# Kernel optimization log

Measured on AMD Instinct MI355X. Metric: run time of the kernel, lower is better.

The kernel has to match this reference:

```python
import jax, jax.numpy as jnp
import numpy as np

K = 3
STRIDE = 1
PAD = 1


def conv2d(x, w, b, stride, pad):
    y = jax.lax.conv_general_dilated(
        x, w, (stride, stride), [(pad, pad), (pad, pad)],
        dimension_numbers=("NCHW", "OIHW", "NCHW"))
    return y + b[None, :, None, None]


def setup_inputs() -> dict:
    key = jax.random.key(0)
    k1, k2, k3, k4, k5, k6 = jax.random.split(key, 6)
    B, C, H, W = 8, 128, 64, 64
    O = 128
    x = jax.random.normal(k1, (B, C, H, W), dtype=jnp.float32)
    # torch zero-inits offset/mask convs; use small random weights so the
    # deformable sampling path is actually exercised (offsets ~O(0.5) px).
    w_offset = jax.random.normal(k2, (2 * K * K, C, K, K), dtype=jnp.float32) * 0.02
    b_offset = jax.random.normal(k3, (2 * K * K,), dtype=jnp.float32) * 0.1
    w_mask = jax.random.normal(k4, (K * K, C, K, K), dtype=jnp.float32) * 0.02
    b_mask = jax.random.normal(k5, (K * K,), dtype=jnp.float32) * 0.1
    fan_in = C * K * K
    bound = 1.0 / np.sqrt(fan_in)  # kaiming_uniform(a=sqrt(5)) bound
    weight = jax.random.uniform(k6, (O, C, K, K), dtype=jnp.float32,
                                minval=-bound, maxval=bound)
    return {"x": x, "w_offset": w_offset, "b_offset": b_offset,
            "w_mask": w_mask, "b_mask": b_mask, "weight": weight}


def deform_conv2d(x, offset, mask, weight):
    B, C, H, W = x.shape
    O = weight.shape[0]
    K2 = K * K
    Ho = (H + 2 * PAD - K) // STRIDE + 1
    Wo = (W + 2 * PAD - K) // STRIDE + 1
    # offset layout: [B, 2*K2, Ho, Wo], per-tap (dy, dx) pairs
    off = offset.reshape(B, K2, 2, Ho, Wo)
    dy, dx = off[:, :, 0], off[:, :, 1]  # [B,K2,Ho,Wo]
    ky, kx = jnp.meshgrid(jnp.arange(K), jnp.arange(K), indexing="ij")
    ky = ky.reshape(K2).astype(jnp.float32)
    kx = kx.reshape(K2).astype(jnp.float32)
    base_y = ky[:, None] + (jnp.arange(Ho, dtype=jnp.float32) * STRIDE - PAD)[None, :]  # [K2,Ho]
    base_x = kx[:, None] + (jnp.arange(Wo, dtype=jnp.float32) * STRIDE - PAD)[None, :]  # [K2,Wo]
    py = dy + base_y[None, :, :, None]  # [B,K2,Ho,Wo]
    px = dx + base_x[None, :, None, :]

    y0 = jnp.floor(py)
    x0 = jnp.floor(px)
    ly = py - y0
    lx = px - x0
    y0i = y0.astype(jnp.int32)
    x0i = x0.astype(jnp.int32)

    xf = x.reshape(B, C, H * W)
    N = K2 * Ho * Wo

    def gather(yi, xi):
        valid = (yi >= 0) & (yi < H) & (xi >= 0) & (xi < W)
        idx = jnp.clip(yi, 0, H - 1) * W + jnp.clip(xi, 0, W - 1)
        v = jnp.take_along_axis(xf, idx.reshape(B, 1, N), axis=2)  # [B,C,N]
        return v * valid.reshape(B, 1, N)

    w00 = ((1 - ly) * (1 - lx)).reshape(B, 1, N)
    w01 = ((1 - ly) * lx).reshape(B, 1, N)
    w10 = (ly * (1 - lx)).reshape(B, 1, N)
    w11 = (ly * lx).reshape(B, 1, N)
    val = (w00 * gather(y0i, x0i) + w01 * gather(y0i, x0i + 1)
           + w10 * gather(y0i + 1, x0i) + w11 * gather(y0i + 1, x0i + 1))  # [B,C,N]
    val = val.reshape(B, C, K2, Ho * Wo) * mask.reshape(B, 1, K2, Ho * Wo)
    out = jnp.einsum("oik,bikn->bon", weight.reshape(O, C, K2), val)
    return out.reshape(B, O, Ho, Wo)


def reference(x, w_offset, b_offset, w_mask, b_mask, weight):
    offset = conv2d(x, w_offset, b_offset, STRIDE, PAD)
    mask = jax.nn.sigmoid(conv2d(x, w_mask, b_mask, STRIDE, PAD))
    return deform_conv2d(x, offset, mask, weight)
```

## Files before the change

kernel.cpp:

```cpp
#include <hip/hip_runtime.h>
#include <hip/hip_fp16.h>
#include <cstdint>

#define B_    8
#define C_    128
#define HW    4096
#define O_    128
#define KDIM  1152

typedef short bf16x8 __attribute__((ext_vector_type(8)));
typedef float f32x4  __attribute__((ext_vector_type(4)));

__device__ __forceinline__ unsigned short f2bf(float f) {
  unsigned u = __float_as_uint(f);
  u += 0x7FFFu + ((u >> 16) & 1u);
  return (unsigned short)(u >> 16);
}
__device__ __forceinline__ float bf_lo(unsigned u) { return __uint_as_float(u << 16); }
__device__ __forceinline__ float bf_hi(unsigned u) { return __uint_as_float(u & 0xFFFF0000u); }

#define WS_WBF   0
#define WS_WCB   294912
#define WS_ZERO  368640
#define WS_XT    368896
#define WS_PW    8757504
#define WS_PA    11116800
#define WS_COUT  12296448

__global__ void k_prep(const float* __restrict__ weight,
                       const float* __restrict__ w_off, const float* __restrict__ w_msk,
                       unsigned short* __restrict__ Wbf, unsigned short* __restrict__ wcb,
                       float* __restrict__ zero) {
  int gid = blockIdx.x * 256 + threadIdx.x;
  if (gid < O_ * KDIM) {
    int o = gid / KDIM, i = gid - o * KDIM;
    int k2 = i >> 7, c = i & 127;
    Wbf[gid] = f2bf(weight[o * KDIM + c * 9 + k2]);
  }
  if (gid < 9 * 32 * 128) {
    int t = gid >> 12, rem = gid & 4095;
    int o = rem >> 7, c = rem & 127;
    float v = 0.f;
    if (o < 18) v = w_off[o * KDIM + c * 9 + t];
    else if (o < 27) v = w_msk[(o - 18) * KDIM + c * 9 + t];
    wcb[gid] = f2bf(v);
  }
  if (gid < 64) zero[gid] = 0.f;
}

__global__ __launch_bounds__(256) void k_xt(const float* __restrict__ x,
                                            unsigned short* __restrict__ xt) {
  __shared__ unsigned short tile[64][130];
  int bid = blockIdx.x;
  int b = bid >> 6, p0 = (bid & 63) << 6;
  int tid = threadIdx.x;
  int pl = tid & 63, cq = tid >> 6;
  const float* xb = x + (size_t)b * C_ * HW + p0 + pl;
#pragma unroll
  for (int i = 0; i < 32; ++i) {
    int c = cq * 32 + i;
    tile[pl][c] = f2bf(xb[(size_t)c * HW]);
  }
  __syncthreads();
  int cd = tid & 63, pr = tid >> 6;
  unsigned* dst = (unsigned*)xt + ((size_t)b * HW + p0) * 64 + cd;
  const unsigned* t32 = (const unsigned*)&tile[0][0];
#pragma unroll
  for (int j = 0; j < 16; ++j) {
    int p = pr + j * 4;
    dst[(size_t)p * 64] = t32[p * 65 + cd];
  }
}

__global__ __launch_bounds__(256) void k_cgemm(const unsigned short* __restrict__ xt,
                                               const unsigned short* __restrict__ wcb,
                                               const float* __restrict__ zero,
                                               float* __restrict__ cout) {
  __shared__ __align__(16) unsigned short As[2][128 * 128];
  __shared__ __align__(16) unsigned short Bs[2][32 * 128];

  int bid = blockIdx.x;
  int b = bid >> 5;
  int p0 = (bid & 31) << 7;
  int tid = threadIdx.x, lane = tid & 63, wv = tid >> 6;
  int lhi = lane >> 4, llo = lane & 15;

  const unsigned short* xb = xt + (size_t)b * HW * C_;

  auto STAGE = [&](int t, int bufi) {
    int ky = t / 3, kx = t - ky * 3;
    int dshift = (ky - 1) * 64 + (kx - 1);
#pragma unroll
    for (int i = 0; i < 8; ++i) {
      int chunk = i * 256 + tid;
      int r = chunk >> 4, j = chunk & 15;
      int p = p0 + r;
      int ho = p >> 6, wo = p & 63;
      int iy = ho + ky - 1, ix = wo + kx - 1;
      bool valid = ((unsigned)iy < 64u) && ((unsigned)ix < 64u);
      int jj = j ^ (r & 15);
      const unsigned short* src = valid ? (xb + (size_t)(p + dshift) * C_ + jj * 8)
                                        : (const unsigned short*)zero;
      __builtin_amdgcn_global_load_lds(
          (const __attribute__((address_space(1))) unsigned*)src,
          (__attribute__((address_space(3))) unsigned*)((char*)&As[bufi][0] + i * 4096 + wv * 1024),
          16, 0, 0);
    }
#pragma unroll
    for (int i = 0; i < 2; ++i) {
      int chunk = i * 256 + tid;
      int o = chunk >> 4, j = chunk & 15;
      int jj = j ^ (o & 15);
      __builtin_amdgcn_global_load_lds(
          (const __attribute__((address_space(1))) unsigned*)(wcb + (size_t)t * 4096 + o * 128 + jj * 8),
          (__attribute__((address_space(3))) unsigned*)((char*)&Bs[bufi][0] + i * 4096 + wv * 1024),
          16, 0, 0);
    }
  };

  f32x4 acc[2][2] = {};
  STAGE(0, 0);
  __syncthreads();
  int buf = 0;
  for (int t = 0; t < 9; ++t) {
    if (t < 8) STAGE(t + 1, buf ^ 1);
    bf16x8 bfv[2][4];
#pragma unroll
    for (int n = 0; n < 2; ++n)
#pragma unroll
      for (int ks = 0; ks < 4; ++ks) {
        int row = n * 16 + llo;
        int off = row * 256 + (((ks * 4 + lhi) ^ (row & 15)) << 4);
        bfv[n][ks] = *(const bf16x8*)((const char*)&Bs[buf][0] + off);
      }
#pragma unroll
    for (int ks = 0; ks < 4; ++ks) {
      bf16x8 af[2];
#pragma unroll
      for (int m = 0; m < 2; ++m) {
        int row = wv * 32 + m * 16 + llo;
        int off = row * 256 + (((ks * 4 + lhi) ^ (row & 15)) << 4);
        af[m] = *(const bf16x8*)((const char*)&As[buf][0] + off);
      }
#pragma unroll
      for (int m = 0; m < 2; ++m)
#pragma unroll
        for (int n = 0; n < 2; ++n)
          acc[m][n] = __builtin_amdgcn_mfma_f32_16x16x32_bf16(af[m], bfv[n][ks], acc[m][n], 0, 0, 0);
    }
    __syncthreads();
    buf ^= 1;
  }

  float* cb = cout + ((size_t)b * HW + p0) * 32;
#pragma unroll
  for (int m = 0; m < 2; ++m)
#pragma unroll
    for (int n = 0; n < 2; ++n)
#pragma unroll
      for (int r = 0; r < 4; ++r) {
        int pix = wv * 32 + m * 16 + lhi * 4 + r;
        int o = n * 16 + llo;
        cb[(size_t)pix * 32 + o] = acc[m][n][r];
      }
}

__global__ __launch_bounds__(256) void k_rp(const float* __restrict__ cout,
                                            const float* __restrict__ b_off,
                                            const float* __restrict__ b_msk,
                                            uint2* __restrict__ pwh,
                                            unsigned* __restrict__ paw) {
  int gid = blockIdx.x * 256 + threadIdx.x;
  int b = gid >> 12, p = gid & 4095;
  const float* cr = cout + (size_t)gid * 32;
  float v[28];
#pragma unroll
  for (int j = 0; j < 7; ++j) *(f32x4*)&v[j * 4] = *(const f32x4*)(cr + j * 4);
  int ho = p >> 6, wo = p & 63;
#pragma unroll
  for (int k2 = 0; k2 < 9; ++k2) {
    int ky = k2 / 3, kx = k2 - ky * 3;
    float dy = v[2 * k2] + b_off[2 * k2];
    float dx = v[2 * k2 + 1] + b_off[2 * k2 + 1];
    float mk = v[18 + k2] + b_msk[k2];
    mk = 1.f / (1.f + __expf(-mk));
    float py = dy + (float)(ho + ky - 1);
    float px = dx + (float)(wo + kx - 1);
    float fy = floorf(py), fx = floorf(px);
    float ly = py - fy, lx = px - fx;
    int y0 = (int)fy, x0 = (int)fx;
    float vy0 = ((unsigned)y0 < 64u) ? 1.f : 0.f;
    float vy1 = ((unsigned)(y0 + 1) < 64u) ? 1.f : 0.f;
    float vx0 = ((unsigned)x0 < 64u) ? 1.f : 0.f;
    float vx1 = ((unsigned)(x0 + 1) < 64u) ? 1.f : 0.f;
    int cy0 = min(max(y0, 0), 63);
    int cx0 = min(max(x0, 0), 63);
    float wy0 = (1.f - ly) * mk, wy1 = ly * mk;
    float w00 = wy0 * (1.f - lx) * vy0 * vx0, w01 = wy0 * lx * vy0 * vx1;
    float w10 = wy1 * (1.f - lx) * vy1 * vx0, w11 = wy1 * lx * vy1 * vx1;
    int dxf = (x0 >= 0 && x0 <= 62) ? 1 : 0;
    int dyf = (y0 >= 0 && y0 <= 62) ? 1 : 0;
    unsigned h00 = __half_as_ushort(__float2half_rn(w00));
    unsigned h01 = __half_as_ushort(__float2half_rn(w01));
    unsigned h10 = __half_as_ushort(__float2half_rn(w10));
    unsigned h11 = __half_as_ushort(__float2half_rn(w11));
    int idx = (b * 9 + k2) * HW + p;
    pwh[idx] = make_uint2(h00 | (h01 << 16), h10 | (h11 << 16));
    paw[idx] = (unsigned)(cy0 * 64 + cx0) | (dxf << 12) | (dyf << 13);
  }
}

__global__ __launch_bounds__(256) void k_fused(const unsigned* __restrict__ xt32,
                                               const uint2* __restrict__ pwh,
                                               const unsigned* __restrict__ paw,
                                               const unsigned short* __restrict__ Wbf,
                                               float* __restrict__ out) {
  __shared__ __align__(16) unsigned short As[2][128 * 64];
  __shared__ __align__(16) unsigned short Bs[2][64 * 128];

  int bid = blockIdx.x;
  int b = bid >> 6;
  int pbase = (bid & 63) << 6;
  int tid = threadIdx.x, lane = tid & 63;
  int wuni = __builtin_amdgcn_readfirstlane(tid >> 6);
  int wr = wuni >> 1, wc = wuni & 1;
  int lhi = lane >> 4, llo = lane & 15;

  const unsigned* xb32 = xt32 + ((size_t)b << 18);

  uint2 Wv[8]; unsigned awv[8]; unsigned g[32];

  auto B_ISSUE = [&](int k2n, int half) {
    int pp0 = wuni * 16 + half * 8;
    int pidx0 = (b * 9 + k2n) * HW + pbase + pp0;
#pragma unroll
    for (int i = 0; i < 8; ++i) { Wv[i] = pwh[pidx0 + i]; awv[i] = paw[pidx0 + i]; }
#pragma unroll
    for (int i = 0; i < 8; ++i) {
      unsigned aw = awv[i];
      unsigned a00 = (aw & 4095u) << 6;
      unsigned dxs = ((aw >> 12) & 1u) << 6;
      unsigned dys = ((aw >> 13) & 1u) << 12;
      g[i * 4 + 0] = xb32[a00 + lane];
      g[i * 4 + 1] = xb32[a00 + dxs + lane];
      g[i * 4 + 2] = xb32[a00 + dys + lane];
      g[i * 4 + 3] = xb32[a00 + dys + dxs + lane];
    }
  };
  auto B_FIN = [&](int bufn, int half) {
#pragma unroll
    for (int i = 0; i < 8; ++i) {
      float2 f0 = __half22float2(*reinterpret_cast<__half2*>(&Wv[i].x));
      float2 f1 = __half22float2(*reinterpret_cast<__half2*>(&Wv[i].y));
      unsigned v00 = g[i*4], v01 = g[i*4+1], v10 = g[i*4+2], v11 = g[i*4+3];
      float lo = f0.x*bf_lo(v00) + f0.y*bf_lo(v01) + f1.x*bf_lo(v10) + f1.y*bf_lo(v11);
      float hi = f0.x*bf_hi(v00) + f0.y*bf_hi(v01) + f1.x*bf_hi(v10) + f1.y*bf_hi(v11);
      unsigned pk = (unsigned)f2bf(lo) | ((unsigned)f2bf(hi) << 16);
      int row = wuni * 16 + half * 8 + i;
      unsigned off = (unsigned)(row * 256) + (((unsigned)lane * 4u) ^ ((unsigned)(row & 7) << 4));
      *(unsigned*)((char*)&Bs[bufn][0] + off) = pk;
    }
  };
  auto STAGE_A = [&](int kt, int abuf) {
#pragma unroll
    for (int j = 0; j < 4; ++j) {
      int chunk = j * 256 + tid;
      int row = chunk >> 3;
      int sch = (chunk & 7) ^ (row & 7);
      __builtin_amdgcn_global_load_lds(
          (const __attribute__((address_space(1))) unsigned*)(Wbf + (size_t)row * KDIM + kt * 64 + sch * 8),
          (__attribute__((address_space(3))) unsigned*)((char*)&As[abuf][0] + j * 4096 + wuni * 1024),
          16, 0, 0);
    }
  };

  f32x4 acc[4][2] = {};
  auto MSTEP = [&](int abuf, int bbuf, int bhalf) {
#pragma unroll
    for (int ks = 0; ks < 2; ++ks) {
      bf16x8 af[4], bfv[2];
#pragma unroll
      for (int m = 0; m < 4; ++m) {
        int row = wr * 64 + m * 16 + llo;
        int off = row * 128 + ((ks * 64 + lhi * 16) ^ ((llo & 7) << 4));
        af[m] = *(const bf16x8*)((const char*)&As[abuf][0] + off);
      }
#pragma unroll
      for (int n = 0; n < 2; ++n) {
        int row = wc * 32 + n * 16 + llo;
        int off = row * 256 + ((bhalf * 128 + ks * 64 + lhi * 16) ^ ((row & 7) << 4));
        bfv[n] = *(const bf16x8*)((const char*)&Bs[bbuf][0] + off);
      }
#pragma unroll
      for (int m = 0; m < 4; ++m)
#pragma unroll
        for (int n = 0; n < 2; ++n)
          acc[m][n] = __builtin_amdgcn_mfma_f32_16x16x32_bf16(af[m], bfv[n], acc[m][n], 0, 0, 0);
    }
  };

  B_ISSUE(0, 0); B_FIN(0, 0);
  B_ISSUE(0, 1); B_FIN(0, 1);
  STAGE_A(0, 0);
  __syncthreads();

  for (int k2 = 0; k2 < 9; ++k2) {
    int kt0 = 2 * k2;
    if (kt0 + 1 < 18) STAGE_A(kt0 + 1, (kt0 + 1) & 1);
    if (k2 < 8) B_ISSUE(k2 + 1, 0);
    MSTEP(kt0 & 1, k2 & 1, 0);
    if (k2 < 8) B_FIN((k2 + 1) & 1, 0);
    __syncthreads();
    if (kt0 + 2 < 18) STAGE_A(kt0 + 2, (kt0 + 2) & 1);
    if (k2 < 8) B_ISSUE(k2 + 1, 1);
    MSTEP((kt0 + 1) & 1, k2 & 1, 1);
    if (k2 < 8) B_FIN((k2 + 1) & 1, 1);
    __syncthreads();
  }

  float* ob = out + (size_t)b * O_ * HW + pbase;
#pragma unroll
  for (int m = 0; m < 4; ++m) {
    int o0 = wr * 64 + m * 16 + lhi * 4;
#pragma unroll
    for (int n = 0; n < 2; ++n) {
      int px = wc * 32 + n * 16 + llo;
#pragma unroll
      for (int r = 0; r < 4; ++r)
        ob[(size_t)(o0 + r) * HW + px] = acc[m][n][r];
    }
  }
}

extern "C" void kernel_launch(void* const* d_in, const int* in_sizes, int n_in,
                              void* d_out, int out_size, void* d_ws, size_t ws_size,
                              hipStream_t stream) {
  const float* x      = (const float*)d_in[0];
  const float* w_off  = (const float*)d_in[1];
  const float* b_off  = (const float*)d_in[2];
  const float* w_msk  = (const float*)d_in[3];
  const float* b_msk  = (const float*)d_in[4];
  const float* weight = (const float*)d_in[5];
  float* out = (float*)d_out;
  char* ws = (char*)d_ws;

  unsigned short* Wbf  = (unsigned short*)(ws + WS_WBF);
  unsigned short* wcb  = (unsigned short*)(ws + WS_WCB);
  float*          zero = (float*)(ws + WS_ZERO);
  unsigned short* xt   = (unsigned short*)(ws + WS_XT);
  uint2*          pwh  = (uint2*)(ws + WS_PW);
  unsigned*       paw  = (unsigned*)(ws + WS_PA);
  float*          cgo  = (float*)(ws + WS_COUT);

  k_prep  <<<576, 256, 0, stream>>>(weight, w_off, w_msk, Wbf, wcb, zero);
  k_xt    <<<512, 256, 0, stream>>>(x, xt);
  k_cgemm <<<256, 256, 0, stream>>>(xt, wcb, zero, cgo);
  k_rp    <<<128, 256, 0, stream>>>(cgo, b_off, b_msk, pwh, paw);
  k_fused <<<512, 256, 0, stream>>>((const unsigned*)xt, pwh, paw, Wbf, out);
}
```

Before: 132.4 us.

## Deepen gather pipeline in fused kernel, merge prep kernels, parallelize offset decode

The fused deformable GEMM now keeps gathered samples for two K-half steps in flight, using a triple-buffered B tile in LDS, explicit vmcnt waits, sched barriers and raised priority around the MFMA block. The two prep kernels (weight conversion and x transpose) are merged into a single launch to save one kernel launch. The offset/mask decode kernel now uses one thread per (batch, tap, pixel) instead of looping over taps, which gives many more blocks. The costs are higher register and LDS pressure in the fused kernel, and fragile hand-written waitcnt counts.

```diff
diff --git a/kernel.cpp b/kernel.cpp
--- a/kernel.cpp
+++ b/kernel.cpp
@@ -27,33 +27,37 @@
 #define WS_PA    11116800
 #define WS_COUT  12296448
 
-__global__ void k_prep(const float* __restrict__ weight,
-                       const float* __restrict__ w_off, const float* __restrict__ w_msk,
-                       unsigned short* __restrict__ Wbf, unsigned short* __restrict__ wcb,
-                       float* __restrict__ zero) {
-  int gid = blockIdx.x * 256 + threadIdx.x;
-  if (gid < O_ * KDIM) {
-    int o = gid / KDIM, i = gid - o * KDIM;
-    int k2 = i >> 7, c = i & 127;
-    Wbf[gid] = f2bf(weight[o * KDIM + c * 9 + k2]);
-  }
-  if (gid < 9 * 32 * 128) {
-    int t = gid >> 12, rem = gid & 4095;
-    int o = rem >> 7, c = rem & 127;
-    float v = 0.f;
-    if (o < 18) v = w_off[o * KDIM + c * 9 + t];
-    else if (o < 27) v = w_msk[(o - 18) * KDIM + c * 9 + t];
-    wcb[gid] = f2bf(v);
-  }
-  if (gid < 64) zero[gid] = 0.f;
-}
-
-__global__ __launch_bounds__(256) void k_xt(const float* __restrict__ x,
+__global__ __launch_bounds__(256) void k_px(const float* __restrict__ weight,
+                                            const float* __restrict__ w_off,
+                                            const float* __restrict__ w_msk,
+                                            const float* __restrict__ x,
+                                            unsigned short* __restrict__ Wbf,
+                                            unsigned short* __restrict__ wcb,
+                                            float* __restrict__ zero,
                                             unsigned short* __restrict__ xt) {
   __shared__ unsigned short tile[64][130];
   int bid = blockIdx.x;
-  int b = bid >> 6, p0 = (bid & 63) << 6;
   int tid = threadIdx.x;
+  if (bid < 576) {
+    int gid = bid * 256 + tid;
+    if (gid < O_ * KDIM) {
+      int o = gid / KDIM, i = gid - o * KDIM;
+      int k2 = i >> 7, c = i & 127;
+      Wbf[gid] = f2bf(weight[o * KDIM + c * 9 + k2]);
+    }
+    if (gid < 9 * 32 * 128) {
+      int t = gid >> 12, rem = gid & 4095;
+      int o = rem >> 7, c = rem & 127;
+      float v = 0.f;
+      if (o < 18) v = w_off[o * KDIM + c * 9 + t];
+      else if (o < 27) v = w_msk[(o - 18) * KDIM + c * 9 + t];
+      wcb[gid] = f2bf(v);
+    }
+    if (gid < 64) zero[gid] = 0.f;
+    return;
+  }
+  int xb_id = bid - 576;
+  int b = xb_id >> 6, p0 = (xb_id & 63) << 6;
   int pl = tid & 63, cq = tid >> 6;
   const float* xb = x + (size_t)b * C_ * HW + p0 + pl;
 #pragma unroll
@@ -171,52 +175,47 @@
                                             uint2* __restrict__ pwh,
                                             unsigned* __restrict__ paw) {
   int gid = blockIdx.x * 256 + threadIdx.x;
-  int b = gid >> 12, p = gid & 4095;
-  const float* cr = cout + (size_t)gid * 32;
-  float v[28];
-#pragma unroll
-  for (int j = 0; j < 7; ++j) *(f32x4*)&v[j * 4] = *(const f32x4*)(cr + j * 4);
+  int p = gid & 4095;
+  int bk = gid >> 12;
+  int b = bk / 9, k2 = bk - 9 * b;
+  const float* cr = cout + ((size_t)b * HW + p) * 32;
+  float dy = cr[2 * k2]     + b_off[2 * k2];
+  float dx = cr[2 * k2 + 1] + b_off[2 * k2 + 1];
+  float mk = cr[18 + k2]    + b_msk[k2];
+  mk = 1.f / (1.f + __expf(-mk));
   int ho = p >> 6, wo = p & 63;
-#pragma unroll
-  for (int k2 = 0; k2 < 9; ++k2) {
-    int ky = k2 / 3, kx = k2 - ky * 3;
-    float dy = v[2 * k2] + b_off[2 * k2];
-    float dx = v[2 * k2 + 1] + b_off[2 * k2 + 1];
-    float mk = v[18 + k2] + b_msk[k2];
-    mk = 1.f / (1.f + __expf(-mk));
-    float py = dy + (float)(ho + ky - 1);
-    float px = dx + (float)(wo + kx - 1);
-    float fy = floorf(py), fx = floorf(px);
-    float ly = py - fy, lx = px - fx;
-    int y0 = (int)fy, x0 = (int)fx;
-    float vy0 = ((unsigned)y0 < 64u) ? 1.f : 0.f;
-    float vy1 = ((unsigned)(y0 + 1) < 64u) ? 1.f : 0.f;
-    float vx0 = ((unsigned)x0 < 64u) ? 1.f : 0.f;
-    float vx1 = ((unsigned)(x0 + 1) < 64u) ? 1.f : 0.f;
-    int cy0 = min(max(y0, 0), 63);
-    int cx0 = min(max(x0, 0), 63);
-    float wy0 = (1.f - ly) * mk, wy1 = ly * mk;
-    float w00 = wy0 * (1.f - lx) * vy0 * vx0, w01 = wy0 * lx * vy0 * vx1;
-    float w10 = wy1 * (1.f - lx) * vy1 * vx0, w11 = wy1 * lx * vy1 * vx1;
-    int dxf = (x0 >= 0 && x0 <= 62) ? 1 : 0;
-    int dyf = (y0 >= 0 && y0 <= 62) ? 1 : 0;
-    unsigned h00 = __half_as_ushort(__float2half_rn(w00));
-    unsigned h01 = __half_as_ushort(__float2half_rn(w01));
-    unsigned h10 = __half_as_ushort(__float2half_rn(w10));
-    unsigned h11 = __half_as_ushort(__float2half_rn(w11));
-    int idx = (b * 9 + k2) * HW + p;
-    pwh[idx] = make_uint2(h00 | (h01 << 16), h10 | (h11 << 16));
-    paw[idx] = (unsigned)(cy0 * 64 + cx0) | (dxf << 12) | (dyf << 13);
-  }
-}
-
-__global__ __launch_bounds__(256) void k_fused(const unsigned* __restrict__ xt32,
-                                               const uint2* __restrict__ pwh,
-                                               const unsigned* __restrict__ paw,
-                                               const unsigned short* __restrict__ Wbf,
-                                               float* __restrict__ out) {
+  int ky = k2 / 3, kx = k2 - ky * 3;
+  float py = dy + (float)(ho + ky - 1);
+  float px = dx + (float)(wo + kx - 1);
+  float fy = floorf(py), fx = floorf(px);
+  float ly = py - fy, lx = px - fx;
+  int y0 = (int)fy, x0 = (int)fx;
+  float vy0 = ((unsigned)y0 < 64u) ? 1.f : 0.f;
+  float vy1 = ((unsigned)(y0 + 1) < 64u) ? 1.f : 0.f;
+  float vx0 = ((unsigned)x0 < 64u) ? 1.f : 0.f;
+  float vx1 = ((unsigned)(x0 + 1) < 64u) ? 1.f : 0.f;
+  int cy0 = min(max(y0, 0), 63);
+  int cx0 = min(max(x0, 0), 63);
+  float wy0 = (1.f - ly) * mk, wy1 = ly * mk;
+  float w00 = wy0 * (1.f - lx) * vy0 * vx0, w01 = wy0 * lx * vy0 * vx1;
+  float w10 = wy1 * (1.f - lx) * vy1 * vx0, w11 = wy1 * lx * vy1 * vx1;
+  int dxf = (x0 >= 0 && x0 <= 62) ? 1 : 0;
+  int dyf = (y0 >= 0 && y0 <= 62) ? 1 : 0;
+  unsigned h00 = __half_as_ushort(__float2half_rn(w00));
+  unsigned h01 = __half_as_ushort(__float2half_rn(w01));
+  unsigned h10 = __half_as_ushort(__float2half_rn(w10));
+  unsigned h11 = __half_as_ushort(__float2half_rn(w11));
+  pwh[gid] = make_uint2(h00 | (h01 << 16), h10 | (h11 << 16));
+  paw[gid] = (unsigned)(cy0 * 64 + cx0) | (dxf << 12) | (dyf << 13);
+}
+
+__global__ __launch_bounds__(256, 2) void k_fused(const unsigned* __restrict__ xt32,
+                                                  const uint2* __restrict__ pwh,
+                                                  const unsigned* __restrict__ paw,
+                                                  const unsigned short* __restrict__ Wbf,
+                                                  float* __restrict__ out) {
   __shared__ __align__(16) unsigned short As[2][128 * 64];
-  __shared__ __align__(16) unsigned short Bs[2][64 * 128];
+  __shared__ __align__(16) unsigned short Bs[3][64 * 128];
 
   int bid = blockIdx.x;
   int b = bid >> 6;
@@ -228,31 +227,33 @@
 
   const unsigned* xb32 = xt32 + ((size_t)b << 18);
 
-  uint2 Wv[8]; unsigned awv[8]; unsigned g[32];
-
-  auto B_ISSUE = [&](int k2n, int half) {
-    int pp0 = wuni * 16 + half * 8;
-    int pidx0 = (b * 9 + k2n) * HW + pbase + pp0;
-#pragma unroll
-    for (int i = 0; i < 8; ++i) { Wv[i] = pwh[pidx0 + i]; awv[i] = paw[pidx0 + i]; }
+  uint2 Wv[2][8]; unsigned Av[2][8]; unsigned g[2][32];
+
+  auto PARAMS = [&](int q, int s) {
+    int tap = q >> 1, half = q & 1;
+    int base = (b * 9 + tap) * HW + pbase + wuni * 16 + half * 8;
+#pragma unroll
+    for (int i = 0; i < 8; ++i) { Wv[s][i] = pwh[base + i]; Av[s][i] = paw[base + i]; }
+  };
+  auto ISSUE = [&](int s) {
 #pragma unroll
     for (int i = 0; i < 8; ++i) {
-      unsigned aw = awv[i];
+      unsigned aw = Av[s][i];
       unsigned a00 = (aw & 4095u) << 6;
       unsigned dxs = ((aw >> 12) & 1u) << 6;
       unsigned dys = ((aw >> 13) & 1u) << 12;
-      g[i * 4 + 0] = xb32[a00 + lane];
-      g[i * 4 + 1] = xb32[a00 + dxs + lane];
-      g[i * 4 + 2] = xb32[a00 + dys + lane];
-      g[i * 4 + 3] = xb32[a00 + dys + dxs + lane];
-    }
-  };
-  auto B_FIN = [&](int bufn, int half) {
+      g[s][i * 4 + 0] = xb32[a00 + lane];
+      g[s][i * 4 + 1] = xb32[a00 + dxs + lane];
+      g[s][i * 4 + 2] = xb32[a00 + dys + lane];
+      g[s][i * 4 + 3] = xb32[a00 + dys + dxs + lane];
+    }
+  };
+  auto FIN = [&](int s, int bufn, int half) {
 #pragma unroll
     for (int i = 0; i < 8; ++i) {
-      float2 f0 = __half22float2(*reinterpret_cast<__half2*>(&Wv[i].x));
-      float2 f1 = __half22float2(*reinterpret_cast<__half2*>(&Wv[i].y));
-      unsigned v00 = g[i*4], v01 = g[i*4+1], v10 = g[i*4+2], v11 = g[i*4+3];
+      float2 f0 = __half22float2(*reinterpret_cast<__half2*>(&Wv[s][i].x));
+      float2 f1 = __half22float2(*reinterpret_cast<__half2*>(&Wv[s][i].y));
+      unsigned v00 = g[s][i*4], v01 = g[s][i*4+1], v10 = g[s][i*4+2], v11 = g[s][i*4+3];
       float lo = f0.x*bf_lo(v00) + f0.y*bf_lo(v01) + f1.x*bf_lo(v10) + f1.y*bf_lo(v11);
       float hi = f0.x*bf_hi(v00) + f0.y*bf_hi(v01) + f1.x*bf_hi(v10) + f1.y*bf_hi(v11);
       unsigned pk = (unsigned)f2bf(lo) | ((unsigned)f2bf(hi) << 16);
@@ -275,7 +276,8 @@
   };
 
   f32x4 acc[4][2] = {};
-  auto MSTEP = [&](int abuf, int bbuf, int bhalf) {
+  auto MSTEP = [&](int abuf, int bbuf, int kh) {
+    __builtin_amdgcn_s_setprio(1);
 #pragma unroll
     for (int ks = 0; ks < 2; ++ks) {
       bf16x8 af[4], bfv[2];
@@ -288,7 +290,7 @@
 #pragma unroll
       for (int n = 0; n < 2; ++n) {
         int row = wc * 32 + n * 16 + llo;
-        int off = row * 256 + ((bhalf * 128 + ks * 64 + lhi * 16) ^ ((row & 7) << 4));
+        int off = row * 256 + ((kh * 128 + ks * 64 + lhi * 16) ^ ((row & 7) << 4));
         bfv[n] = *(const bf16x8*)((const char*)&Bs[bbuf][0] + off);
       }
 #pragma unroll
@@ -297,25 +299,34 @@
         for (int n = 0; n < 2; ++n)
           acc[m][n] = __builtin_amdgcn_mfma_f32_16x16x32_bf16(af[m], bfv[n], acc[m][n], 0, 0, 0);
     }
-  };
-
-  B_ISSUE(0, 0); B_FIN(0, 0);
-  B_ISSUE(0, 1); B_FIN(0, 1);
+    __builtin_amdgcn_s_setprio(0);
+  };
+
+  PARAMS(0, 0); PARAMS(1, 1);
+  ISSUE(0); ISSUE(1);
+  FIN(0, 0, 0);
+  PARAMS(2, 0);
+  FIN(1, 0, 1);
+  PARAMS(3, 1);
+  ISSUE(0);
   STAGE_A(0, 0);
   __syncthreads();
 
-  for (int k2 = 0; k2 < 9; ++k2) {
-    int kt0 = 2 * k2;
-    if (kt0 + 1 < 18) STAGE_A(kt0 + 1, (kt0 + 1) & 1);
-    if (k2 < 8) B_ISSUE(k2 + 1, 0);
-    MSTEP(kt0 & 1, k2 & 1, 0);
-    if (k2 < 8) B_FIN((k2 + 1) & 1, 0);
-    __syncthreads();
-    if (kt0 + 2 < 18) STAGE_A(kt0 + 2, (kt0 + 2) & 1);
-    if (k2 < 8) B_ISSUE(k2 + 1, 1);
-    MSTEP((kt0 + 1) & 1, k2 & 1, 1);
-    if (k2 < 8) B_FIN((k2 + 1) & 1, 1);
-    __syncthreads();
+#pragma unroll 6
+  for (int p = 0; p < 18; ++p) {
+    if (p + 1 < 18) STAGE_A(p + 1, (p + 1) & 1);
+    __builtin_amdgcn_sched_barrier(0);
+    if (p + 3 < 18) ISSUE((p + 1) & 1);
+    MSTEP(p & 1, ((p >> 1) % 3), p & 1);
+    if (p + 2 < 18) FIN(p & 1, (((p + 2) >> 1) % 3), p & 1);
+    if (p + 4 < 18) PARAMS(p + 4, p & 1);
+    if (p < 17) {
+      if (p <= 14) asm volatile("s_waitcnt vmcnt(32)" ::: "memory");
+      else         asm volatile("s_waitcnt vmcnt(0)"  ::: "memory");
+      asm volatile("s_waitcnt lgkmcnt(0)" ::: "memory");
+      __builtin_amdgcn_s_barrier();
+      __builtin_amdgcn_sched_barrier(0);
+    }
   }
 
   float* ob = out + (size_t)b * O_ * HW + pbase;
@@ -352,9 +363,8 @@
   unsigned*       paw  = (unsigned*)(ws + WS_PA);
   float*          cgo  = (float*)(ws + WS_COUT);
 
-  k_prep  <<<576, 256, 0, stream>>>(weight, w_off, w_msk, Wbf, wcb, zero);
-  k_xt    <<<512, 256, 0, stream>>>(x, xt);
+  k_px    <<<1088, 256, 0, stream>>>(weight, w_off, w_msk, x, Wbf, wcb, zero, xt);
   k_cgemm <<<256, 256, 0, stream>>>(xt, wcb, zero, cgo);
-  k_rp    <<<128, 256, 0, stream>>>(cgo, b_off, b_msk, pwh, paw);
+  k_rp    <<<1152, 256, 0, stream>>>(cgo, b_off, b_msk, pwh, paw);
   k_fused <<<512, 256, 0, stream>>>((const unsigned*)xt, pwh, paw, Wbf, out);
 }
```

After: 131.8 us. Within noise of the previous version (-0.4%).
